# Kernel optimization log

Hardware: AMD Instinct MI355X
Metric: run time of the kernel (lower is better)

Reference implementation:

```python
import jax, jax.numpy as jnp
import numpy as np

N = 50000          # number of nodes
NNZ = 800000       # edges per relation (avg degree 16)
R = 3              # edge_features / number of relations
D_IN = 128
D_OUT = 128
EPS = 1e-6


def setup_inputs() -> dict:
    key = jax.random.key(0)
    ks = jax.random.split(key, 8)
    return {
        "input": jax.random.normal(ks[0], (N, D_IN), dtype=jnp.float32),
        "adj_rows": jax.random.randint(ks[1], (R, NNZ), 0, N, dtype=jnp.int64) if jax.config.jax_enable_x64 else jax.random.randint(ks[1], (R, NNZ), 0, N).astype(jnp.int32),
        "adj_cols": jax.random.randint(ks[2], (R, NNZ), 0, N, dtype=jnp.int64) if jax.config.jax_enable_x64 else jax.random.randint(ks[2], (R, NNZ), 0, N).astype(jnp.int32),
        "adj_vals": jax.random.uniform(ks[3], (R, NNZ), dtype=jnp.float32),
        "weight": jax.random.normal(ks[4], (D_IN * R, D_OUT), dtype=jnp.float32) * (1.0 / np.sqrt(D_OUT)),
        "share_weight": jax.random.normal(ks[5], (D_IN, D_OUT), dtype=jnp.float32) * (1.0 / np.sqrt(D_OUT)),
        "bias": jax.random.normal(ks[6], (D_OUT,), dtype=jnp.float32) * (1.0 / np.sqrt(D_OUT)),
        "ln_gamma": jnp.ones((D_IN,), dtype=jnp.float32),
        "ln_beta": jnp.zeros((D_IN,), dtype=jnp.float32),
    }


def _spmm(rows, cols, vals, x, n_nodes):
    # (sparse A) @ x via gather + segment-sum: out[r] = sum_{e: rows[e]=r} vals[e]*x[cols[e]]
    msgs = vals[:, None] * x[cols]            # [nnz, d]
    return jax.ops.segment_sum(msgs, rows, num_segments=n_nodes)


def _layernorm(x, gamma, beta):
    mu = jnp.mean(x, axis=-1, keepdims=True)
    var = jnp.var(x, axis=-1, keepdims=True)
    return (x - mu) * jax.lax.rsqrt(var + EPS) * gamma + beta


def reference(input, adj_rows, adj_cols, adj_vals, weight, share_weight, bias, ln_gamma, ln_beta):
    n = input.shape[0]
    # loop over the small fixed relation set to keep peak memory low
    support_list = [
        _spmm(adj_rows[r], adj_cols[r], adj_vals[r], input, n) for r in range(adj_rows.shape[0])
    ]
    support = jnp.concatenate(support_list, axis=1)   # [N, R*d_in]
    support_sum = support_list[0]
    for s in support_list[1:]:
        support_sum = support_sum + s
    support_norm = _layernorm(support_sum, ln_gamma, ln_beta)
    out = (support @ weight + support_norm @ share_weight) * 0.5
    return out + bias
```

## Files before the change

kernel.cpp:

```cpp
#include <hip/hip_runtime.h>
#include <hip/hip_fp16.h>

constexpr int NN  = 50000;
constexpr int NNZ = 800000;
constexpr int RR  = 3;
constexpr int D   = 128;
constexpr int RN  = RR * NN;
constexpr int NE  = RR * NNZ;
constexpr int KK  = 512;
constexpr int MPAD = 50048;
constexpr int PART = 256;
constexpr int PSZ  = (RN + PART - 1) / PART;
constexpr int CAP  = 10240;
constexpr int EPB  = 2048;
constexpr int CAPB = 24;
constexpr float EPS = 1e-6f;

using bf16x8 = __attribute__((ext_vector_type(8))) __bf16;
using f32x4  = __attribute__((ext_vector_type(4))) float;

__device__ __forceinline__ unsigned pack_bf2(float a, float b) {
  unsigned ua = __float_as_uint(a); ua = (ua + (0x7FFFu + ((ua >> 16) & 1))) >> 16;
  unsigned ub = __float_as_uint(b); ub = (ub + (0x7FFFu + ((ub >> 16) & 1))) >> 16;
  return ua | (ub << 16);
}
__device__ __forceinline__ unsigned bf16_lo(float a) {
  unsigned ua = __float_as_uint(a);
  return (ua + (0x7FFFu + ((ua >> 16) & 1))) >> 16;
}

__device__ __forceinline__ void gload16(const void* g, void* l) {
  __builtin_amdgcn_global_load_lds(
      (const __attribute__((address_space(1))) unsigned int*)g,
      (__attribute__((address_space(3))) unsigned int*)l, 16, 0, 0);
}

#define ACC2(accA, accB, word, vv) {                                   \
    __half2 _h = __builtin_bit_cast(__half2, (word));                  \
    accA = __builtin_fmaf(__half2float(_h.x), (vv), accA);             \
    accB = __builtin_fmaf(__half2float(_h.y), (vv), accB); }

__device__ __forceinline__ float val16(unsigned u) {
  return __half2float(__ushort_as_half((unsigned short)(u & 0xFFFFu)));
}

__global__ __launch_bounds__(256) void part_split(
    const int*   __restrict__ rows,
    const int*   __restrict__ cols,
    const float* __restrict__ vals,
    int* __restrict__ pcur,
    uint2* __restrict__ pedges) {
  __shared__ int lcur[PART], lbase[PART];
  __shared__ uint2 lbuf[PART][CAPB];
  int t = threadIdx.x;
  lcur[t] = 0;
  __syncthreads();
  int e0 = blockIdx.x * EPB;
  constexpr int EPT = EPB / 256;
  int ovf_pe[EPT], ovf_rank[EPT];
  uint2 ovf_val[EPT];
  #pragma unroll
  for (int j = 0; j < EPT; j++) {
    ovf_pe[j] = -1;
    int e = e0 + j * 256 + t;
    if (e < NE) {
      int r = (e >= 2 * NNZ) ? 2 : (e >= NNZ ? 1 : 0);
      int b = r * NN + rows[e];
      int p = b / PSZ;
      unsigned pay = ((unsigned)cols[e] << 16) |
                     (unsigned)__half_as_ushort(__float2half_rn(vals[e]));
      int rank = atomicAdd(&lcur[p], 1);
      if (rank < CAPB) {
        lbuf[p][rank] = make_uint2((unsigned)b, pay);
      } else {
        ovf_pe[j] = p; ovf_rank[j] = rank;
        ovf_val[j] = make_uint2((unsigned)b, pay);
      }
    }
  }
  __syncthreads();
  lbase[t] = atomicAdd(&pcur[t], lcur[t]);
  __syncthreads();
  int wid = t >> 6, l = t & 63;
  for (int q = 0; q < 64; q++) {
    int p = wid * 64 + q;
    int n = min(lcur[p], CAPB);
    uint2* dst = pedges + (size_t)p * CAP + lbase[p];
    for (int i = l; i < n; i += 64) dst[i] = lbuf[p][i];
  }
  #pragma unroll
  for (int j = 0; j < EPT; j++)
    if (ovf_pe[j] >= 0)
      pedges[(size_t)ovf_pe[j] * CAP + lbase[ovf_pe[j]] + ovf_rank[j]] = ovf_val[j];
}

__global__ __launch_bounds__(64) void psum(
    const int* __restrict__ pcur, int* __restrict__ pbase, int* __restrict__ off) {
  int l = threadIdx.x;
  int carry = 0;
  for (int base = 0; base < PART; base += 64) {
    int v = pcur[base + l];
    int inc = v;
    #pragma unroll
    for (int s = 1; s < 64; s <<= 1) {
      int u = __shfl_up(inc, s);
      if (l >= s) inc += u;
    }
    pbase[base + l] = inc - v + carry;
    carry += __shfl(inc, 63);
  }
  if (l == 0) off[RN] = NE;
}

__global__ __launch_bounds__(256) void sort_part(
    const uint2* __restrict__ pedges,
    const int*   __restrict__ pcur,
    const int*   __restrict__ pbase,
    int* __restrict__ off,
    unsigned* __restrict__ epack) {
  __shared__ int sc[PSZ];
  __shared__ int sdata[256];
  int p = blockIdx.x;
  int t = threadIdx.x;
  int bb = p * PSZ;
  int nbuck = min(PSZ, RN - bb);
  int n = pcur[p];
  int gbase = pbase[p];
  const uint2* src = pedges + (size_t)p * CAP;

  for (int i = t; i < nbuck; i += 256) sc[i] = 0;
  __syncthreads();
  for (int i = t; i < n; i += 256)
    atomicAdd(&sc[src[i].x - bb], 1);
  __syncthreads();

  constexpr int PER = (PSZ + 255) / 256;
  int lo = t * PER, hi = min(lo + PER, nbuck);
  int s = 0;
  for (int i = lo; i < hi; i++) s += sc[i];
  sdata[t] = s;
  __syncthreads();
  #pragma unroll
  for (int step = 1; step < 256; step <<= 1) {
    int v = (t >= step) ? sdata[t - step] : 0;
    __syncthreads();
    sdata[t] += v;
    __syncthreads();
  }
  int run = gbase + sdata[t] - s;
  for (int i = lo; i < hi; i++) {
    int c = sc[i];
    sc[i] = run;
    off[bb + i] = run;
    run += c;
  }
  __syncthreads();

  for (int i = t; i < n; i += 256) {
    uint2 ed = src[i];
    int pos = atomicAdd(&sc[ed.x - bb], 1);
    epack[pos] = ed.y;
  }
}

__global__ __launch_bounds__(256) void build_xh(
    const float* __restrict__ x, unsigned* __restrict__ xh) {
  int i = blockIdx.x * 256 + threadIdx.x;
  if (i >= NN * 64) return;
  float2 v = ((const float2*)x)[i];
  xh[i] = __builtin_bit_cast(unsigned, __floats2half2_rn(v.x, v.y));
}

__global__ __launch_bounds__(256) void gather_ln(
    const unsigned* __restrict__ xh,
    const unsigned* __restrict__ epack,
    const int*      __restrict__ off,
    const float* __restrict__ gamma,
    const float* __restrict__ beta,
    unsigned* __restrict__ Au) {
  int node = blockIdx.x * 4 + (threadIdx.x >> 6);
  if (node >= NN) return;
  int lane = threadIdx.x & 63;
  int g  = lane >> 4;
  int q  = lane & 15;
  const unsigned* xq = xh + q * 4;

  float l0=0,l1=0,l2=0,l3=0,l4=0,l5=0,l6=0,l7=0;

  #pragma unroll
  for (int r = 0; r < RR; r++) {
    int b = r * NN + node;
    int s = off[b], e2 = off[b + 1];
    float a0=0,a1=0,a2=0,a3=0,a4=0,a5=0,a6=0,a7=0;

    for (int i0 = s; i0 < e2; i0 += 64) {
      int navail = min(64, e2 - i0);
      unsigned ep = (lane < navail) ? epack[i0 + lane] : 0u;
      int c0 = 0;
      for (; c0 + 16 <= navail; c0 += 16) {
        unsigned ua = __shfl(ep, c0 + g);
        unsigned ub = __shfl(ep, c0 + 4 + g);
        unsigned uc = __shfl(ep, c0 + 8 + g);
        unsigned ud = __shfl(ep, c0 + 12 + g);
        uint4 ga = *(const uint4*)(xq + (size_t)(ua >> 16) * 64);
        uint4 gb = *(const uint4*)(xq + (size_t)(ub >> 16) * 64);
        uint4 gc = *(const uint4*)(xq + (size_t)(uc >> 16) * 64);
        uint4 gd = *(const uint4*)(xq + (size_t)(ud >> 16) * 64);
        float va = val16(ua), vb = val16(ub), vc = val16(uc), vd = val16(ud);
        ACC2(a0,a1,ga.x,va) ACC2(a2,a3,ga.y,va) ACC2(a4,a5,ga.z,va) ACC2(a6,a7,ga.w,va)
        ACC2(a0,a1,gb.x,vb) ACC2(a2,a3,gb.y,vb) ACC2(a4,a5,gb.z,vb) ACC2(a6,a7,gb.w,vb)
        ACC2(a0,a1,gc.x,vc) ACC2(a2,a3,gc.y,vc) ACC2(a4,a5,gc.z,vc) ACC2(a6,a7,gc.w,vc)
        ACC2(a0,a1,gd.x,vd) ACC2(a2,a3,gd.y,vd) ACC2(a4,a5,gd.z,vd) ACC2(a6,a7,gd.w,vd)
      }
      for (; c0 + 8 <= navail; c0 += 8) {
        unsigned ua = __shfl(ep, c0 + g);
        unsigned ub = __shfl(ep, c0 + 4 + g);
        uint4 ga = *(const uint4*)(xq + (size_t)(ua >> 16) * 64);
        uint4 gb = *(const uint4*)(xq + (size_t)(ub >> 16) * 64);
        float va = val16(ua), vb = val16(ub);
        ACC2(a0,a1,ga.x,va) ACC2(a2,a3,ga.y,va) ACC2(a4,a5,ga.z,va) ACC2(a6,a7,ga.w,va)
        ACC2(a0,a1,gb.x,vb) ACC2(a2,a3,gb.y,vb) ACC2(a4,a5,gb.z,vb) ACC2(a6,a7,gb.w,vb)
      }
      for (; c0 < navail; c0 += 4) {
        int eidx = c0 + g;
        unsigned u = __shfl(ep, min(eidx, navail - 1));
        float v = (eidx < navail) ? val16(u) : 0.0f;
        uint4 gg = *(const uint4*)(xq + (size_t)(u >> 16) * 64);
        ACC2(a0,a1,gg.x,v) ACC2(a2,a3,gg.y,v) ACC2(a4,a5,gg.z,v) ACC2(a6,a7,gg.w,v)
      }
    }
    #define REDG(x) x += __shfl_xor(x, 16); x += __shfl_xor(x, 32);
    REDG(a0) REDG(a1) REDG(a2) REDG(a3) REDG(a4) REDG(a5) REDG(a6) REDG(a7)
    #undef REDG
    if (g == 0) {
      uint4 w;
      w.x = pack_bf2(a0, a1); w.y = pack_bf2(a2, a3);
      w.z = pack_bf2(a4, a5); w.w = pack_bf2(a6, a7);
      *(uint4*)(Au + (size_t)node * 256 + r * 64 + q * 4) = w;
    }
    l0 += a0; l1 += a1; l2 += a2; l3 += a3;
    l4 += a4; l5 += a5; l6 += a6; l7 += a7;
  }

  float sum = l0+l1+l2+l3+l4+l5+l6+l7;
  float sq  = l0*l0+l1*l1+l2*l2+l3*l3+l4*l4+l5*l5+l6*l6+l7*l7;
  #pragma unroll
  for (int m = 1; m <= 8; m <<= 1) {
    sum += __shfl_xor(sum, m);
    sq  += __shfl_xor(sq,  m);
  }
  float mean = sum * (1.0f / D);
  float var  = sq * (1.0f / D) - mean * mean;
  float rstd = rsqrtf(var + EPS);
  float4 gm0 = *(const float4*)&gamma[8 * q];
  float4 gm1 = *(const float4*)&gamma[8 * q + 4];
  float4 bt0 = *(const float4*)&beta[8 * q];
  float4 bt1 = *(const float4*)&beta[8 * q + 4];
  float o0 = (l0 - mean) * rstd * gm0.x + bt0.x;
  float o1 = (l1 - mean) * rstd * gm0.y + bt0.y;
  float o2 = (l2 - mean) * rstd * gm0.z + bt0.z;
  float o3 = (l3 - mean) * rstd * gm0.w + bt0.w;
  float o4 = (l4 - mean) * rstd * gm1.x + bt1.x;
  float o5 = (l5 - mean) * rstd * gm1.y + bt1.y;
  float o6 = (l6 - mean) * rstd * gm1.z + bt1.z;
  float o7 = (l7 - mean) * rstd * gm1.w + bt1.w;
  if (g == 0) {
    uint4 w;
    w.x = pack_bf2(o0, o1); w.y = pack_bf2(o2, o3);
    w.z = pack_bf2(o4, o5); w.w = pack_bf2(o6, o7);
    *(uint4*)(Au + (size_t)node * 256 + 192 + q * 4) = w;
  }
}

__global__ __launch_bounds__(256) void build_wt(
    const float* __restrict__ w,
    const float* __restrict__ shw,
    unsigned short* __restrict__ WT) {
  int idx = blockIdx.x * 256 + threadIdx.x;
  int k   = idx >> 7;
  int col = idx & 127;
  float v = (k < 384) ? w[k * 128 + col] : shw[(k - 384) * 128 + col];
  WT[col * 512 + k] = (unsigned short)bf16_lo(v);
}

__global__ __launch_bounds__(256) void gemm_mfma(
    const char* __restrict__ Ab,
    const char* __restrict__ Bb,
    const float* __restrict__ bias,
    float* __restrict__ out) {
  __shared__ __align__(16) char smem[24576];
  char* As = smem;
  char* Bs = smem + 8192;

  int tid  = threadIdx.x;
  int wid  = tid >> 6;
  int lane = tid & 63;
  int wr   = wid >> 1;
  int wc   = wid & 1;
  int row0 = blockIdx.x * 64;

  f32x4 zero = {0.f, 0.f, 0.f, 0.f};
  f32x4 acc[2][4];
  #pragma unroll
  for (int i = 0; i < 2; i++)
    #pragma unroll
    for (int j = 0; j < 4; j++) acc[i][j] = zero;

  for (int kc = 0; kc < 8; kc++) {
    #pragma unroll
    for (int i = 0; i < 2; i++) {
      int c = i * 256 + tid;
      int r = c >> 3, s = c & 7;
      int ss = s ^ (r & 7);
      const void* src = Ab + (size_t)(row0 + r) * 1024 + kc * 128 + ss * 16;
      void* dst = As + i * 4096 + wid * 1024;
      gload16(src, dst);
    }
    #pragma unroll
    for (int i = 0; i < 4; i++) {
      int c = i * 256 + tid;
      int r = c >> 3, s = c & 7;
      int ss = s ^ (r & 7);
      const void* src = Bb + (size_t)r * 1024 + kc * 128 + ss * 16;
      void* dst = Bs + i * 4096 + wid * 1024;
      gload16(src, dst);
    }
    __syncthreads();

    #pragma unroll
    for (int ks = 0; ks < 2; ks++) {
      bf16x8 afrag[2], bfrag[4];
      int sg = ks * 4 + (lane >> 4);
      #pragma unroll
      for (int rb = 0; rb < 2; rb++) {
        int r = wr * 32 + rb * 16 + (lane & 15);
        afrag[rb] = *(const bf16x8*)(As + r * 128 + (sg ^ (r & 7)) * 16);
      }
      #pragma unroll
      for (int cb = 0; cb < 4; cb++) {
        int col = wc * 64 + cb * 16 + (lane & 15);
        bfrag[cb] = *(const bf16x8*)(Bs + col * 128 + (sg ^ (col & 7)) * 16);
      }
      #pragma unroll
      for (int rb = 0; rb < 2; rb++)
        #pragma unroll
        for (int cb = 0; cb < 4; cb++)
          acc[rb][cb] = __builtin_amdgcn_mfma_f32_16x16x32_bf16(
              afrag[rb], bfrag[cb], acc[rb][cb], 0, 0, 0);
    }
    __syncthreads();
  }

  #pragma unroll
  for (int rb = 0; rb < 2; rb++) {
    #pragma unroll
    for (int cb = 0; cb < 4; cb++) {
      int col = wc * 64 + cb * 16 + (lane & 15);
      float bv = bias[col];
      #pragma unroll
      for (int r = 0; r < 4; r++) {
        int grow = row0 + wr * 32 + rb * 16 + (lane >> 4) * 4 + r;
        if (grow < NN) out[(size_t)grow * 128 + col] = 0.5f * acc[rb][cb][r] + bv;
      }
    }
  }
}

extern "C" void kernel_launch(void* const* d_in, const int* in_sizes, int n_in,
                              void* d_out, int out_size, void* d_ws, size_t ws_size,
                              hipStream_t stream) {
  const float* input  = (const float*)d_in[0];
  const int*   arows  = (const int*)  d_in[1];
  const int*   acols  = (const int*)  d_in[2];
  const float* avals  = (const float*)d_in[3];
  const float* weight = (const float*)d_in[4];
  const float* shw    = (const float*)d_in[5];
  const float* bias   = (const float*)d_in[6];
  const float* gamma  = (const float*)d_in[7];
  const float* beta   = (const float*)d_in[8];
  float* out = (float*)d_out;

  char* ws = (char*)d_ws;
  char*  Abf   = ws;                         ws += (size_t)MPAD * KK * 2;
  unsigned short* WT = (unsigned short*)ws;  ws += (size_t)128 * KK * 2;
  unsigned* xh  = (unsigned*)ws;             ws += (size_t)NN * 64 * 4;
  uint2* pedges = (uint2*)ws;                ws += (size_t)PART * CAP * sizeof(uint2);
  unsigned* epack = (unsigned*)ws;           ws += (size_t)NE * 4;
  int*   off   = (int*)ws;                   ws += ((size_t)RN + 4) * sizeof(int);
  int*   pcur  = (int*)ws;                   ws += (size_t)PART * sizeof(int);
  int*   pbase = (int*)ws;                   ws += (size_t)PART * sizeof(int);

  hipMemsetAsync(pcur, 0, (size_t)PART * sizeof(int), stream);
  build_wt   <<<256, 256, 0, stream>>>(weight, shw, WT);
  build_xh   <<<(NN * 64 + 255) / 256, 256, 0, stream>>>(input, xh);
  part_split <<<(NE + EPB - 1) / EPB, 256, 0, stream>>>(arows, acols, avals,
                                                        pcur, pedges);
  psum       <<<1, 64, 0, stream>>>(pcur, pbase, off);
  sort_part  <<<PART, 256, 0, stream>>>(pedges, pcur, pbase, off, epack);
  gather_ln  <<<(NN + 3) / 4, 256, 0, stream>>>(xh, epack, off, gamma, beta,
                                                (unsigned*)Abf);
  gemm_mfma  <<<MPAD / 64, 256, 0, stream>>>(Abf, (const char*)WT, bias, out);
}
```

Baseline: 187.5 us.

## Merge preprocessing kernels, fold prefix scan into sort, and widen GEMM tile

Fuses the weight-transpose, fp16 conversion of x and edge partitioning into one `prep` launch, with blocks split by block index. The separate `psum` kernel is removed: each `sort_part` block now computes its own partition base by reducing the `pcur` counts of earlier partitions. The gather tail drops its 8-edge step, and the GEMM now uses 128-row tiles with 512 threads, so B is loaded once per 128 rows instead of once per 64. The aim is to cut launch count and inter-kernel gaps and to reuse B tiles better; the costs are a redundant per-block reduction and a larger LDS footprint per GEMM block.

Result: faster. 178.7 us (-4.7%).

```diff
diff --git a/kernel.cpp b/kernel.cpp
--- a/kernel.cpp
+++ b/kernel.cpp
@@ -16,6 +16,10 @@
 constexpr int CAPB = 24;
 constexpr float EPS = 1e-6f;
 
+constexpr int NB_SPLIT = (NE + EPB - 1) / EPB;
+constexpr int NB_XH    = (NN * 64 + 255) / 256;
+constexpr int NB_WT    = 256;
+
 using bf16x8 = __attribute__((ext_vector_type(8))) __bf16;
 using f32x4  = __attribute__((ext_vector_type(4))) float;
 
@@ -35,27 +39,50 @@
       (__attribute__((address_space(3))) unsigned int*)l, 16, 0, 0);
 }
 
+__device__ __forceinline__ float val16(unsigned u) {
+  return __half2float(__ushort_as_half((unsigned short)(u & 0xFFFFu)));
+}
+
 #define ACC2(accA, accB, word, vv) {                                   \
     __half2 _h = __builtin_bit_cast(__half2, (word));                  \
     accA = __builtin_fmaf(__half2float(_h.x), (vv), accA);             \
     accB = __builtin_fmaf(__half2float(_h.y), (vv), accB); }
 
-__device__ __forceinline__ float val16(unsigned u) {
-  return __half2float(__ushort_as_half((unsigned short)(u & 0xFFFFu)));
-}
-
-__global__ __launch_bounds__(256) void part_split(
+__global__ __launch_bounds__(256) void prep(
     const int*   __restrict__ rows,
     const int*   __restrict__ cols,
     const float* __restrict__ vals,
-    int* __restrict__ pcur,
-    uint2* __restrict__ pedges) {
+    const float* __restrict__ x,
+    const float* __restrict__ w,
+    const float* __restrict__ shw,
+    int*   __restrict__ pcur,
+    uint2* __restrict__ pedges,
+    unsigned* __restrict__ xh,
+    unsigned short* __restrict__ WT) {
   __shared__ int lcur[PART], lbase[PART];
   __shared__ uint2 lbuf[PART][CAPB];
+  int blk = blockIdx.x;
   int t = threadIdx.x;
+
+  if (blk >= NB_SPLIT) {
+    int b2 = blk - NB_SPLIT;
+    if (b2 < NB_XH) {
+      int i = b2 * 256 + t;
+      float2 v = ((const float2*)x)[i];
+      xh[i] = __builtin_bit_cast(unsigned, __floats2half2_rn(v.x, v.y));
+    } else {
+      int idx = (b2 - NB_XH) * 256 + t;
+      int k   = idx >> 7;
+      int col = idx & 127;
+      float v = (k < 384) ? w[k * 128 + col] : shw[(k - 384) * 128 + col];
+      WT[col * 512 + k] = (unsigned short)bf16_lo(v);
+    }
+    return;
+  }
+
   lcur[t] = 0;
   __syncthreads();
-  int e0 = blockIdx.x * EPB;
+  int e0 = blk * EPB;
   constexpr int EPT = EPB / 256;
   int ovf_pe[EPT], ovf_rank[EPT];
   uint2 ovf_val[EPT];
@@ -94,28 +121,9 @@
       pedges[(size_t)ovf_pe[j] * CAP + lbase[ovf_pe[j]] + ovf_rank[j]] = ovf_val[j];
 }
 
-__global__ __launch_bounds__(64) void psum(
-    const int* __restrict__ pcur, int* __restrict__ pbase, int* __restrict__ off) {
-  int l = threadIdx.x;
-  int carry = 0;
-  for (int base = 0; base < PART; base += 64) {
-    int v = pcur[base + l];
-    int inc = v;
-    #pragma unroll
-    for (int s = 1; s < 64; s <<= 1) {
-      int u = __shfl_up(inc, s);
-      if (l >= s) inc += u;
-    }
-    pbase[base + l] = inc - v + carry;
-    carry += __shfl(inc, 63);
-  }
-  if (l == 0) off[RN] = NE;
-}
-
 __global__ __launch_bounds__(256) void sort_part(
     const uint2* __restrict__ pedges,
     const int*   __restrict__ pcur,
-    const int*   __restrict__ pbase,
     int* __restrict__ off,
     unsigned* __restrict__ epack) {
   __shared__ int sc[PSZ];
@@ -125,8 +133,18 @@
   int bb = p * PSZ;
   int nbuck = min(PSZ, RN - bb);
   int n = pcur[p];
-  int gbase = pbase[p];
   const uint2* src = pedges + (size_t)p * CAP;
+
+  sdata[t] = (t < p) ? pcur[t] : 0;
+  __syncthreads();
+  #pragma unroll
+  for (int step = 128; step >= 1; step >>= 1) {
+    if (t < step) sdata[t] += sdata[t + step];
+    __syncthreads();
+  }
+  int gbase = sdata[0];
+  __syncthreads();
+  if (p == 0 && t == 0) off[RN] = NE;
 
   for (int i = t; i < nbuck; i += 256) sc[i] = 0;
   __syncthreads();
@@ -161,14 +179,6 @@
     int pos = atomicAdd(&sc[ed.x - bb], 1);
     epack[pos] = ed.y;
   }
-}
-
-__global__ __launch_bounds__(256) void build_xh(
-    const float* __restrict__ x, unsigned* __restrict__ xh) {
-  int i = blockIdx.x * 256 + threadIdx.x;
-  if (i >= NN * 64) return;
-  float2 v = ((const float2*)x)[i];
-  xh[i] = __builtin_bit_cast(unsigned, __floats2half2_rn(v.x, v.y));
 }
 
 __global__ __launch_bounds__(256) void gather_ln(
@@ -212,16 +222,13 @@
         ACC2(a0,a1,gc.x,vc) ACC2(a2,a3,gc.y,vc) ACC2(a4,a5,gc.z,vc) ACC2(a6,a7,gc.w,vc)
         ACC2(a0,a1,gd.x,vd) ACC2(a2,a3,gd.y,vd) ACC2(a4,a5,gd.z,vd) ACC2(a6,a7,gd.w,vd)
       }
-      for (; c0 + 8 <= navail; c0 += 8) {
-        unsigned ua = __shfl(ep, c0 + g);
-        unsigned ub = __shfl(ep, c0 + 4 + g);
-        uint4 ga = *(const uint4*)(xq + (size_t)(ua >> 16) * 64);
-        uint4 gb = *(const uint4*)(xq + (size_t)(ub >> 16) * 64);
-        float va = val16(ua), vb = val16(ub);
-        ACC2(a0,a1,ga.x,va) ACC2(a2,a3,ga.y,va) ACC2(a4,a5,ga.z,va) ACC2(a6,a7,ga.w,va)
-        ACC2(a0,a1,gb.x,vb) ACC2(a2,a3,gb.y,vb) ACC2(a4,a5,gb.z,vb) ACC2(a6,a7,gb.w,vb)
-      }
-      for (; c0 < navail; c0 += 4) {
+      for (; c0 + 4 <= navail; c0 += 4) {
+        unsigned u = __shfl(ep, c0 + g);
+        uint4 gg = *(const uint4*)(xq + (size_t)(u >> 16) * 64);
+        float v = val16(u);
+        ACC2(a0,a1,gg.x,v) ACC2(a2,a3,gg.y,v) ACC2(a4,a5,gg.z,v) ACC2(a6,a7,gg.w,v)
+      }
+      if (c0 < navail) {
         int eidx = c0 + g;
         unsigned u = __shfl(ep, min(eidx, navail - 1));
         float v = (eidx < navail) ? val16(u) : 0.0f;
@@ -272,32 +279,21 @@
   }
 }
 
-__global__ __launch_bounds__(256) void build_wt(
-    const float* __restrict__ w,
-    const float* __restrict__ shw,
-    unsigned short* __restrict__ WT) {
-  int idx = blockIdx.x * 256 + threadIdx.x;
-  int k   = idx >> 7;
-  int col = idx & 127;
-  float v = (k < 384) ? w[k * 128 + col] : shw[(k - 384) * 128 + col];
-  WT[col * 512 + k] = (unsigned short)bf16_lo(v);
-}
-
-__global__ __launch_bounds__(256) void gemm_mfma(
+__global__ __launch_bounds__(512) void gemm_mfma(
     const char* __restrict__ Ab,
     const char* __restrict__ Bb,
     const float* __restrict__ bias,
     float* __restrict__ out) {
-  __shared__ __align__(16) char smem[24576];
+  __shared__ __align__(16) char smem[32768];
   char* As = smem;
-  char* Bs = smem + 8192;
+  char* Bs = smem + 16384;
 
   int tid  = threadIdx.x;
   int wid  = tid >> 6;
   int lane = tid & 63;
   int wr   = wid >> 1;
   int wc   = wid & 1;
-  int row0 = blockIdx.x * 64;
+  int row0 = blockIdx.x * 128;
 
   f32x4 zero = {0.f, 0.f, 0.f, 0.f};
   f32x4 acc[2][4];
@@ -309,20 +305,20 @@
   for (int kc = 0; kc < 8; kc++) {
     #pragma unroll
     for (int i = 0; i < 2; i++) {
-      int c = i * 256 + tid;
+      int c = i * 512 + tid;
       int r = c >> 3, s = c & 7;
       int ss = s ^ (r & 7);
       const void* src = Ab + (size_t)(row0 + r) * 1024 + kc * 128 + ss * 16;
-      void* dst = As + i * 4096 + wid * 1024;
+      void* dst = As + i * 8192 + wid * 1024;
       gload16(src, dst);
     }
     #pragma unroll
-    for (int i = 0; i < 4; i++) {
-      int c = i * 256 + tid;
+    for (int i = 0; i < 2; i++) {
+      int c = i * 512 + tid;
       int r = c >> 3, s = c & 7;
       int ss = s ^ (r & 7);
       const void* src = Bb + (size_t)r * 1024 + kc * 128 + ss * 16;
-      void* dst = Bs + i * 4096 + wid * 1024;
+      void* dst = Bs + i * 8192 + wid * 1024;
       gload16(src, dst);
     }
     __syncthreads();
@@ -388,16 +384,12 @@
   unsigned* epack = (unsigned*)ws;           ws += (size_t)NE * 4;
   int*   off   = (int*)ws;                   ws += ((size_t)RN + 4) * sizeof(int);
   int*   pcur  = (int*)ws;                   ws += (size_t)PART * sizeof(int);
-  int*   pbase = (int*)ws;                   ws += (size_t)PART * sizeof(int);
 
   hipMemsetAsync(pcur, 0, (size_t)PART * sizeof(int), stream);
-  build_wt   <<<256, 256, 0, stream>>>(weight, shw, WT);
-  build_xh   <<<(NN * 64 + 255) / 256, 256, 0, stream>>>(input, xh);
-  part_split <<<(NE + EPB - 1) / EPB, 256, 0, stream>>>(arows, acols, avals,
-                                                        pcur, pedges);
-  psum       <<<1, 64, 0, stream>>>(pcur, pbase, off);
-  sort_part  <<<PART, 256, 0, stream>>>(pedges, pcur, pbase, off, epack);
-  gather_ln  <<<(NN + 3) / 4, 256, 0, stream>>>(xh, epack, off, gamma, beta,
-                                                (unsigned*)Abf);
-  gemm_mfma  <<<MPAD / 64, 256, 0, stream>>>(Abf, (const char*)WT, bias, out);
-}
+  prep      <<<NB_SPLIT + NB_XH + NB_WT, 256, 0, stream>>>(
+                arows, acols, avals, input, weight, shw, pcur, pedges, xh, WT);
+  sort_part <<<PART, 256, 0, stream>>>(pedges, pcur, off, epack);
+  gather_ln <<<(NN + 3) / 4, 256, 0, stream>>>(xh, epack, off, gamma, beta,
+                                               (unsigned*)Abf);
+  gemm_mfma <<<MPAD / 128, 512, 0, stream>>>(Abf, (const char*)WT, bias, out);
+}
```
